# Optimization experiments

Hardware: AMD Instinct MI355X
Metric: run time of the kernel (lower is better)

The kernel has to match this reference:

```python
import jax, jax.numpy as jnp
import numpy as np

N_NODES = 50000
BN_EPS = 1e-5


def sage_conv(x, src, dst, Wl, Wr, b):
    # mean-aggregate neighbor features: message from src -> dst
    msg = x[src]                                             # [E, Din]
    s = jax.ops.segment_sum(msg, dst, num_segments=N_NODES)  # [N, Din]
    cnt = jax.ops.segment_sum(jnp.ones((src.shape[0],), x.dtype), dst,
                              num_segments=N_NODES)          # [N]
    mean = s / jnp.maximum(cnt, 1.0)[:, None]
    # PyG SAGEConv: lin_l(aggregated) (+bias) + lin_r(self), root_weight=True
    return mean @ Wl + b + x @ Wr


def batch_norm(x, gamma, beta):
    mu = jnp.mean(x, axis=0)
    var = jnp.var(x, axis=0)
    return (x - mu) * jax.lax.rsqrt(var + BN_EPS) * gamma + beta


def setup_inputs() -> dict:
    key = jax.random.key(0)
    ks = jax.random.split(key, 16)
    D_IN, D_H, D_OUT = 128, 128, 64
    x = jax.random.normal(ks[0], (N_NODES, D_IN), dtype=jnp.float32)
    edge_index = jax.random.randint(ks[1], (2, 800000), 0, N_NODES, dtype=jnp.int32)

    def xavier(k, din, dout):
        lim = float(np.sqrt(6.0 / (din + dout)))
        return jax.random.uniform(k, (din, dout), jnp.float32, -lim, lim)

    return {
        "x": x, "edge_index": edge_index,
        "Wl0": xavier(ks[2], D_IN, D_H), "Wr0": xavier(ks[3], D_IN, D_H),
        "b0": jnp.zeros((D_H,), jnp.float32),
        "g0": jnp.ones((D_H,), jnp.float32), "be0": jnp.zeros((D_H,), jnp.float32),
        "Wl1": xavier(ks[4], D_H, D_H), "Wr1": xavier(ks[5], D_H, D_H),
        "b1": jnp.zeros((D_H,), jnp.float32),
        "g1": jnp.ones((D_H,), jnp.float32), "be1": jnp.zeros((D_H,), jnp.float32),
        "Wl2": xavier(ks[6], D_H, D_OUT), "Wr2": xavier(ks[7], D_H, D_OUT),
        "b2": jnp.zeros((D_OUT,), jnp.float32),
    }


def reference(x, edge_index, Wl0, Wr0, b0, g0, be0,
              Wl1, Wr1, b1, g1, be1, Wl2, Wr2, b2):
    src, dst = edge_index[0], edge_index[1]
    h = sage_conv(x, src, dst, Wl0, Wr0, b0)
    h = jax.nn.relu(batch_norm(h, g0, be0))
    h = sage_conv(h, src, dst, Wl1, Wr1, b1)
    h = jax.nn.relu(batch_norm(h, g1, be1))
    h = sage_conv(h, src, dst, Wl2, Wr2, b2)
    return jax.nn.log_softmax(h, axis=-1)
```

## Files before the change

kernel.cpp:

```cpp
#include <hip/hip_runtime.h>
#include <hip/hip_bf16.h>

#define D_IN 128
#define D_OUT 64
#define BN_EPS 1e-5f
#define NB_PART 512

typedef short short8 __attribute__((ext_vector_type(8)));
typedef float f32x4 __attribute__((ext_vector_type(4)));
typedef float f32x2 __attribute__((ext_vector_type(2)));
typedef unsigned int u32x4 __attribute__((ext_vector_type(4)));
typedef unsigned int u32x2 __attribute__((ext_vector_type(2)));
typedef unsigned short ushort_t;
typedef unsigned int uint_t;

__device__ __forceinline__ float bf16lo(uint_t v) { return __uint_as_float(v << 16); }
__device__ __forceinline__ float bf16hi(uint_t v) { return __uint_as_float(v & 0xffff0000u); }
__device__ __forceinline__ float bf2f(ushort_t u) { return __uint_as_float(((uint_t)u) << 16); }
__device__ __forceinline__ ushort_t f2bf(float f) {
    union { __hip_bfloat16 h; ushort_t u; } cv;
    cv.h = __float2bfloat16(f);
    return cv.u;
}
__device__ __forceinline__ f32x4 ntload4(const float* p) {
    return __builtin_nontemporal_load((const f32x4*)p);
}


__global__ void hist_kernel(const int* __restrict__ dst, int* __restrict__ cnt, int E) {
    int i = blockIdx.x * 256 + threadIdx.x;
    if (i < E) atomicAdd(&cnt[__builtin_nontemporal_load(&dst[i])], 1);
}

__global__ void scan_part_kernel(const int* __restrict__ cnt, int* __restrict__ bsum, int n) {
    int i = blockIdx.x * 256 + threadIdx.x;
    int v = (i < n) ? cnt[i] : 0;
#pragma unroll
    for (int off = 1; off < 64; off <<= 1) v += __shfl_xor(v, off);
    __shared__ int ws[4];
    int lane = threadIdx.x & 63, wid = threadIdx.x >> 6;
    if (lane == 0) ws[wid] = v;
    __syncthreads();
    if (threadIdx.x == 0) bsum[blockIdx.x] = ws[0] + ws[1] + ws[2] + ws[3];
}

__global__ void scan_mid_kernel(const int* __restrict__ bsum, int* __restrict__ bpre,
                                int* __restrict__ offs, int PB, int n) {
    int t = threadIdx.x;
    int v = (t < PB) ? bsum[t] : 0;
    int lane = t & 63, wid = t >> 6;
    int sc = v;
#pragma unroll
    for (int off = 1; off < 64; off <<= 1) {
        int u = __shfl_up(sc, off);
        if (lane >= off) sc += u;
    }
    __shared__ int ws[4];
    if (lane == 63) ws[wid] = sc;
    __syncthreads();
    int wb = 0;
    for (int w = 0; w < 4; w++) if (w < wid) wb += ws[w];
    int incl = sc + wb;
    if (t < PB) bpre[t] = incl - v;
    if (t == PB - 1) offs[n] = incl;
}

__global__ void scan_final_kernel(const int* __restrict__ cnt, const int* __restrict__ bpre,
                                  int* __restrict__ offs, int* __restrict__ cursor, int n) {
    int b = blockIdx.x, t = threadIdx.x;
    int i = b * 256 + t;
    int v = (i < n) ? cnt[i] : 0;
    int lane = t & 63, wid = t >> 6;
    int sc = v;
#pragma unroll
    for (int off = 1; off < 64; off <<= 1) {
        int u = __shfl_up(sc, off);
        if (lane >= off) sc += u;
    }
    __shared__ int ws[4];
    if (lane == 63) ws[wid] = sc;
    __syncthreads();
    int wb = 0;
    for (int w = 0; w < 4; w++) if (w < wid) wb += ws[w];
    if (i < n) {
        int e = bpre[b] + wb + sc - v;
        offs[i] = e;
        cursor[i] = e;
    }
}

__global__ void scatter_kernel(const int* __restrict__ src, const int* __restrict__ dst,
                               int* __restrict__ cursor, ushort_t* __restrict__ sorted_src,
                               int E, int passW) {
    int lo = blockIdx.y * passW, hi = lo + passW;
    int i = blockIdx.x * 256 + threadIdx.x;
    if (i < E) {
        int d = __builtin_nontemporal_load(&dst[i]);
        if (d >= lo && d < hi) {
            int s = __builtin_nontemporal_load(&src[i]);
            int p = atomicAdd(&cursor[d], 1);
            sorted_src[p] = (ushort_t)s;
        }
    }
}


__global__ void wswz_kernel(const float* __restrict__ Wl0, const float* __restrict__ Wr0,
                            const float* __restrict__ Wl1, const float* __restrict__ Wr1,
                            const float* __restrict__ Wl2, const float* __restrict__ Wr2,
                            short* __restrict__ o0l, short* __restrict__ o0r,
                            short* __restrict__ o1l, short* __restrict__ o1r,
                            short* __restrict__ o2l, short* __restrict__ o2r,
                            int* __restrict__ cnt, int N) {
    int fb = blockIdx.x + 8 * (blockIdx.y + 2 * blockIdx.z);
    for (int i = fb * 256 + threadIdx.x; i < N; i += 48 * 256) cnt[i] = 0;

    int layer = blockIdx.z;
    int Nn = (layer == 2) ? 64 : 128;
    const float* W;
    short* out;
    if (layer == 0) { W = blockIdx.y ? Wr0 : Wl0; out = blockIdx.y ? o0r : o0l; }
    else if (layer == 1) { W = blockIdx.y ? Wr1 : Wl1; out = blockIdx.y ? o1r : o1l; }
    else { W = blockIdx.y ? Wr2 : Wl2; out = blockIdx.y ? o2r : o2l; }
    int g = blockIdx.x * 256 + threadIdx.x;
    int nchunks = (Nn / 16) * 4;
    int chunk = g >> 6, lane = g & 63;
    if (chunk >= nchunks) return;
    int nf = chunk >> 2, kk = chunk & 3;
    short8 s;
#pragma unroll
    for (int j = 0; j < 8; j++) {
        float v = W[(size_t)(kk * 32 + (lane >> 4) * 8 + j) * Nn + nf * 16 + (lane & 15)];
        s[j] = (short)f2bf(v);
    }
    *(short8*)&out[((size_t)(chunk << 6) + lane) * 8] = s;
}


template <int TN, bool BF16IN>
__global__ __launch_bounds__(TN == 128 ? 256 : 128)
void gemm2_mfma(const void* __restrict__ Ain, const short* __restrict__ WlF,
                const short* __restrict__ WrF, ushort_t* __restrict__ Yb,
                ushort_t* __restrict__ Zb, const float* __restrict__ stats,
                const float* __restrict__ gamma, const float* __restrict__ beta, int M) {
    __shared__ short As[64 * 136];
    __shared__ float sc[128], sh[128];
    const int tid = threadIdx.x;
    const int lane = tid & 63;
    const int w = tid >> 6;
    const int row0 = blockIdx.x * 64;
    const int NT = (TN == 128) ? 256 : 128;

    if (BF16IN) {
        if (tid < 128) {
            float invM = 1.0f / (float)M;
            float mu = stats[tid] * invM;
            float var = stats[128 + tid] * invM - mu * mu;
            float scale = gamma[tid] * rsqrtf(var + BN_EPS);
            sc[tid] = scale;
            sh[tid] = beta[tid] - mu * scale;
        }
        __syncthreads();
    }

    for (int c = tid; c < 1024; c += NT) {
        int r = c >> 4, off = (c & 15) * 8;
        short8 v8 = {0, 0, 0, 0, 0, 0, 0, 0};
        if (row0 + r < M) {
            if (BF16IN) {
                const ushort_t* ap = (const ushort_t*)Ain + (size_t)(row0 + r) * 128 + off;
                short8 h = *(const short8*)ap;
#pragma unroll
                for (int j = 0; j < 8; j++) {
                    float f = bf2f((ushort_t)h[j]);
                    f = fmaxf(f * sc[off + j] + sh[off + j], 0.f);
                    v8[j] = (short)f2bf(f);
                }
            } else {
                const float* ap = (const float*)Ain + (size_t)(row0 + r) * 128 + off;
                f32x4 f0 = ntload4(ap);
                f32x4 f1 = ntload4(ap + 4);
#pragma unroll
                for (int j = 0; j < 4; j++) {
                    v8[j] = (short)f2bf(f0[j]);
                    v8[4 + j] = (short)f2bf(f1[j]);
                }
            }
        }
        *(short8*)&As[r * 136 + off] = v8;
    }
    __syncthreads();

    const short* WF;
    ushort_t* D;
    int col0;
    if (TN == 128) {
        bool isY = (w < 2);
        WF = isY ? WlF : WrF;
        D = isY ? Yb : Zb;
        col0 = (w & 1) * 64;
    } else {
        bool isY = (w == 0);
        WF = isY ? WlF : WrF;
        D = isY ? Yb : Zb;
        col0 = 0;
    }

    short8 a[4][4];
#pragma unroll
    for (int m = 0; m < 4; m++)
#pragma unroll
        for (int kk = 0; kk < 4; kk++)
            a[m][kk] = *(const short8*)&As[(m * 16 + (lane & 15)) * 136 + kk * 32 + (lane >> 4) * 8];

    f32x4 acc[4][4];
#pragma unroll
    for (int m = 0; m < 4; m++)
#pragma unroll
        for (int n = 0; n < 4; n++) acc[m][n] = (f32x4){0.f, 0.f, 0.f, 0.f};

#pragma unroll
    for (int kk = 0; kk < 4; kk++) {
#pragma unroll
        for (int n = 0; n < 4; n++) {
            short8 b = *(const short8*)&WF[(size_t)(((col0 >> 4) + n) * 4 + kk) * 512 + lane * 8];
#pragma unroll
            for (int m = 0; m < 4; m++)
                acc[m][n] = __builtin_amdgcn_mfma_f32_16x16x32_bf16(a[m][kk], b, acc[m][n], 0, 0, 0);
        }
    }

#pragma unroll
    for (int m = 0; m < 4; m++) {
#pragma unroll
        for (int i = 0; i < 4; i++) {
            int gr = row0 + m * 16 + (lane >> 4) * 4 + i;
            if (gr < M) {
#pragma unroll
                for (int n = 0; n < 4; n++)
                    D[(size_t)gr * TN + col0 + n * 16 + (lane & 15)] = f2bf(acc[m][n][i]);
            }
        }
    }
}


__global__ __launch_bounds__(256) void agg128_kernel(const ushort_t* __restrict__ Yb,
                                                     const int* __restrict__ offs,
                                                     const ushort_t* __restrict__ sorted_src,
                                                     const float* __restrict__ bias,
                                                     const ushort_t* __restrict__ Zb,
                                                     ushort_t* __restrict__ Hb, int N) {
    int wv = blockIdx.x * 4 + (threadIdx.x >> 6);
    int lane = threadIdx.x & 63;
    int half = lane >> 5, l = lane & 31;
    int node = wv * 2 + half;
    if (node >= N) return;
    int s0 = offs[node], s1 = offs[node + 1];
    float a0 = 0.f, a1 = 0.f, a2 = 0.f, a3 = 0.f;
    int k = s0;
    for (; k + 16 <= s1; k += 16) {
        int idx[16];
#pragma unroll
        for (int j = 0; j < 16; j++) idx[j] = __builtin_nontemporal_load(&sorted_src[k + j]);
        u32x2 v[16];
#pragma unroll
        for (int j = 0; j < 16; j++) v[j] = *(const u32x2*)&Yb[(size_t)idx[j] * 128 + l * 4];
#pragma unroll
        for (int j = 0; j < 16; j++) {
            a0 += bf16lo(v[j][0]);
            a1 += bf16hi(v[j][0]);
            a2 += bf16lo(v[j][1]);
            a3 += bf16hi(v[j][1]);
        }
    }
    for (; k + 4 <= s1; k += 4) {
        int idx[4];
#pragma unroll
        for (int j = 0; j < 4; j++) idx[j] = __builtin_nontemporal_load(&sorted_src[k + j]);
#pragma unroll
        for (int j = 0; j < 4; j++) {
            u32x2 v = *(const u32x2*)&Yb[(size_t)idx[j] * 128 + l * 4];
            a0 += bf16lo(v[0]);
            a1 += bf16hi(v[0]);
            a2 += bf16lo(v[1]);
            a3 += bf16hi(v[1]);
        }
    }
    for (; k < s1; k++) {
        u32x2 v = *(const u32x2*)&Yb[(size_t)sorted_src[k] * 128 + l * 4];
        a0 += bf16lo(v[0]);
        a1 += bf16hi(v[0]);
        a2 += bf16lo(v[1]);
        a3 += bf16hi(v[1]);
    }
    float inv = 1.0f / fmaxf((float)(s1 - s0), 1.0f);
    float4 bb = *(const float4*)&bias[l * 4];
    u32x2 z = __builtin_nontemporal_load((const u32x2*)&Zb[(size_t)node * 128 + l * 4]);
    float h0 = bf16lo(z[0]) + a0 * inv + bb.x;
    float h1 = bf16hi(z[0]) + a1 * inv + bb.y;
    float h2 = bf16lo(z[1]) + a2 * inv + bb.z;
    float h3 = bf16hi(z[1]) + a3 * inv + bb.w;
    u32x2 o;
    o[0] = (uint_t)f2bf(h0) | ((uint_t)f2bf(h1) << 16);
    o[1] = (uint_t)f2bf(h2) | ((uint_t)f2bf(h3) << 16);
    __builtin_nontemporal_store(o, (u32x2*)&Hb[(size_t)node * 128 + l * 4]);
}


__global__ __launch_bounds__(256) void agg_lsm_kernel(const ushort_t* __restrict__ Yb,
                                                      const int* __restrict__ offs,
                                                      const ushort_t* __restrict__ sorted_src,
                                                      const float* __restrict__ bias,
                                                      const ushort_t* __restrict__ Zb,
                                                      float* __restrict__ out, int N) {
    int wv = blockIdx.x * 4 + (threadIdx.x >> 6);
    int lane = threadIdx.x & 63;
    int half = lane >> 5, l = lane & 31;
    int node = wv * 2 + half;
    if (node >= N) return;
    int s0 = offs[node], s1 = offs[node + 1];
    float a0 = 0.f, a1 = 0.f;
    int k = s0;
    for (; k + 8 <= s1; k += 8) {
        int idx[8];
#pragma unroll
        for (int j = 0; j < 8; j++) idx[j] = __builtin_nontemporal_load(&sorted_src[k + j]);
        uint_t v[8];
#pragma unroll
        for (int j = 0; j < 8; j++) v[j] = *(const uint_t*)&Yb[(size_t)idx[j] * 64 + l * 2];
#pragma unroll
        for (int j = 0; j < 8; j++) {
            a0 += bf16lo(v[j]);
            a1 += bf16hi(v[j]);
        }
    }
    for (; k + 4 <= s1; k += 4) {
        int idx[4];
#pragma unroll
        for (int j = 0; j < 4; j++) idx[j] = __builtin_nontemporal_load(&sorted_src[k + j]);
#pragma unroll
        for (int j = 0; j < 4; j++) {
            uint_t v = *(const uint_t*)&Yb[(size_t)idx[j] * 64 + l * 2];
            a0 += bf16lo(v);
            a1 += bf16hi(v);
        }
    }
    for (; k < s1; k++) {
        uint_t v = *(const uint_t*)&Yb[(size_t)sorted_src[k] * 64 + l * 2];
        a0 += bf16lo(v);
        a1 += bf16hi(v);
    }
    float inv = 1.0f / fmaxf((float)(s1 - s0), 1.0f);
    uint_t z = *(const uint_t*)&Zb[(size_t)node * 64 + l * 2];
    float2 bb = *(const float2*)&bias[l * 2];
    float v0 = bf16lo(z) + a0 * inv + bb.x;
    float v1 = bf16hi(z) + a1 * inv + bb.y;
    float m = fmaxf(v0, v1);
#pragma unroll
    for (int off = 16; off; off >>= 1) m = fmaxf(m, __shfl_xor(m, off));
    float s = expf(v0 - m) + expf(v1 - m);
#pragma unroll
    for (int off = 16; off; off >>= 1) s += __shfl_xor(s, off);
    float ls = logf(s);
    f32x2 o;
    o[0] = v0 - m - ls;
    o[1] = v1 - m - ls;
    __builtin_nontemporal_store(o, (f32x2*)&out[(size_t)node * 64 + l * 2]);
}


__global__ __launch_bounds__(256) void bn_part_kernel(const ushort_t* __restrict__ Hb,
                                                      float* __restrict__ P, int M) {
    int b = blockIdx.x;
    int R = (M + NB_PART - 1) / NB_PART;
    int r0 = b * R, r1 = min(r0 + R, M);
    int colg = (threadIdx.x & 15) * 8;
    int rowoff = threadIdx.x >> 4;
    float s[8], s2[8];
#pragma unroll
    for (int j = 0; j < 8; j++) { s[j] = 0.f; s2[j] = 0.f; }
    for (int r = r0 + rowoff; r < r1; r += 16) {
        u32x4 v = __builtin_nontemporal_load((const u32x4*)&Hb[(size_t)r * 128 + colg]);
#pragma unroll
        for (int q = 0; q < 4; q++) {
            float flo = bf16lo(v[q]);
            float fhi = bf16hi(v[q]);
            s[2 * q] += flo;
            s2[2 * q] += flo * flo;
            s[2 * q + 1] += fhi;
            s2[2 * q + 1] += fhi * fhi;
        }
    }
    __shared__ float ls[256][16];
#pragma unroll
    for (int j = 0; j < 8; j++) {
        ls[threadIdx.x][j] = s[j];
        ls[threadIdx.x][8 + j] = s2[j];
    }
    __syncthreads();
    if (threadIdx.x < 128) {
        int g = threadIdx.x >> 3, j = threadIdx.x & 7;
        float a = 0.f, c = 0.f;
#pragma unroll
        for (int kk = 0; kk < 16; kk++) {
            int id = kk * 16 + g;
            a += ls[id][j];
            c += ls[id][8 + j];
        }
        P[(size_t)b * 256 + threadIdx.x] = a;
        P[(size_t)b * 256 + 128 + threadIdx.x] = c;
    }
}

__global__ __launch_bounds__(1024) void bn_reduce_kernel(const float* __restrict__ P,
                                                         float* __restrict__ stats) {
    int c = threadIdx.x & 255, q = threadIdx.x >> 8;
    float acc = 0.f;
#pragma unroll 8
    for (int i = q * (NB_PART / 4); i < (q + 1) * (NB_PART / 4); i++)
        acc += P[(size_t)i * 256 + c];
    __shared__ float ls[4][256];
    ls[q][c] = acc;
    __syncthreads();
    if (threadIdx.x < 256) stats[c] = ls[0][c] + ls[1][c] + ls[2][c] + ls[3][c];
}


extern "C" void kernel_launch(void* const* d_in, const int* in_sizes, int n_in,
                              void* d_out, int out_size, void* d_ws, size_t ws_size,
                              hipStream_t stream) {
    const float* x   = (const float*)d_in[0];
    const int*   ei  = (const int*)d_in[1];
    const float* Wl0 = (const float*)d_in[2];
    const float* Wr0 = (const float*)d_in[3];
    const float* b0  = (const float*)d_in[4];
    const float* g0  = (const float*)d_in[5];
    const float* be0 = (const float*)d_in[6];
    const float* Wl1 = (const float*)d_in[7];
    const float* Wr1 = (const float*)d_in[8];
    const float* b1  = (const float*)d_in[9];
    const float* g1  = (const float*)d_in[10];
    const float* be1 = (const float*)d_in[11];
    const float* Wl2 = (const float*)d_in[12];
    const float* Wr2 = (const float*)d_in[13];
    const float* b2  = (const float*)d_in[14];

    const int N = in_sizes[0] / D_IN;
    const int E = in_sizes[1] / 2;
    const int PB = (N + 255) / 256;

    ushort_t* Hb = (ushort_t*)d_ws;
    ushort_t* Zb = Hb + (size_t)N * D_IN;
    ushort_t* Yb = Zb + (size_t)N * D_IN;
    int* cnt    = (int*)(Yb + (size_t)N * D_IN);
    int* offs   = cnt + N;
    int* cursor = offs + N + 1;
    int* bsum   = cursor + N;
    int* bpre   = bsum + 256;
    ushort_t* sorted = (ushort_t*)(bpre + 256);
    float* stats = (float*)(sorted + E + (E & 1));
    float* P = stats + 512;
    short* WlF0 = (short*)(P + NB_PART * 256);
    short* WrF0 = WlF0 + 16384;
    short* WlF1 = WrF0 + 16384;
    short* WrF1 = WlF1 + 16384;
    short* WlF2 = WrF1 + 16384;
    short* WrF2 = WlF2 + 8192;

    const int eb = (E + 255) / 256;

    wswz_kernel<<<dim3(8, 2, 3), 256, 0, stream>>>(Wl0, Wr0, Wl1, Wr1, Wl2, Wr2,
                                                   WlF0, WrF0, WlF1, WrF1, WlF2, WrF2,
                                                   cnt, N);

    hist_kernel<<<eb, 256, 0, stream>>>(ei + E, cnt, E);
    scan_part_kernel<<<PB, 256, 0, stream>>>(cnt, bsum, N);
    scan_mid_kernel<<<1, 256, 0, stream>>>(bsum, bpre, offs, PB, N);
    scan_final_kernel<<<PB, 256, 0, stream>>>(cnt, bpre, offs, cursor, N);
    scatter_kernel<<<dim3(eb, 2), 256, 0, stream>>>(ei, ei + E, cursor, sorted, E, (N + 1) / 2);

    const int gb = (N + 63) / 64;
    const int ab = (N + 7) / 8;

    gemm2_mfma<128, false><<<gb, 256, 0, stream>>>(x, WlF0, WrF0, Yb, Zb,
                                                   nullptr, nullptr, nullptr, N);
    agg128_kernel<<<ab, 256, 0, stream>>>(Yb, offs, sorted, b0, Zb, Hb, N);
    bn_part_kernel<<<NB_PART, 256, 0, stream>>>(Hb, P, N);
    bn_reduce_kernel<<<1, 1024, 0, stream>>>(P, stats);

    gemm2_mfma<128, true><<<gb, 256, 0, stream>>>(Hb, WlF1, WrF1, Yb, Zb,
                                                  stats, g0, be0, N);
    agg128_kernel<<<ab, 256, 0, stream>>>(Yb, offs, sorted, b1, Zb, Hb, N);
    bn_part_kernel<<<NB_PART, 256, 0, stream>>>(Hb, P, N);
    bn_reduce_kernel<<<1, 1024, 0, stream>>>(P, stats + 256);

    gemm2_mfma<64, true><<<gb, 128, 0, stream>>>(Hb, WlF2, WrF2, Yb, Zb,
                                                 stats + 256, g1, be1, N);
    agg_lsm_kernel<<<ab, 256, 0, stream>>>(Yb, offs, sorted, b2, Zb, (float*)d_out, N);
}
```

Before: 346.4 us.

## Split 128-wide aggregation into column halves across adjacent blocks

The 128-column neighbor aggregation now splits each node's columns into two 64-column halves handled by separate blocks. Block ids are interleaved so that the two halves for the same group of nodes run in adjacent blocks, with each lane loading 4 bytes per neighbor instead of 8. This doubles the number of waves and gives more gather parallelism and latency hiding, and it aims to keep each gathered row half hot in cache for its partner block. The cost is that the index and offset reads are duplicated, and the narrower per-lane loads issue more memory instructions per byte.

```diff
diff --git a/kernel.cpp b/kernel.cpp
--- a/kernel.cpp
+++ b/kernel.cpp
@@ -251,27 +251,30 @@
                                                      const float* __restrict__ bias,
                                                      const ushort_t* __restrict__ Zb,
                                                      ushort_t* __restrict__ Hb, int N) {
-    int wv = blockIdx.x * 4 + (threadIdx.x >> 6);
+    int bid = blockIdx.x;
+    int x = bid & 7;
+    int colhalf = x >> 2;
+    int ng = (bid >> 3) * 4 + (x & 3);
+    int wv = ng * 4 + (threadIdx.x >> 6);
     int lane = threadIdx.x & 63;
     int half = lane >> 5, l = lane & 31;
     int node = wv * 2 + half;
     if (node >= N) return;
+    int cb = colhalf * 64 + l * 2;
     int s0 = offs[node], s1 = offs[node + 1];
-    float a0 = 0.f, a1 = 0.f, a2 = 0.f, a3 = 0.f;
+    float a0 = 0.f, a1 = 0.f;
     int k = s0;
     for (; k + 16 <= s1; k += 16) {
         int idx[16];
 #pragma unroll
         for (int j = 0; j < 16; j++) idx[j] = __builtin_nontemporal_load(&sorted_src[k + j]);
-        u32x2 v[16];
-#pragma unroll
-        for (int j = 0; j < 16; j++) v[j] = *(const u32x2*)&Yb[(size_t)idx[j] * 128 + l * 4];
+        uint_t v[16];
+#pragma unroll
+        for (int j = 0; j < 16; j++) v[j] = *(const uint_t*)&Yb[(size_t)idx[j] * 128 + cb];
 #pragma unroll
         for (int j = 0; j < 16; j++) {
-            a0 += bf16lo(v[j][0]);
-            a1 += bf16hi(v[j][0]);
-            a2 += bf16lo(v[j][1]);
-            a3 += bf16hi(v[j][1]);
+            a0 += bf16lo(v[j]);
+            a1 += bf16hi(v[j]);
         }
     }
     for (; k + 4 <= s1; k += 4) {
@@ -280,31 +283,23 @@
         for (int j = 0; j < 4; j++) idx[j] = __builtin_nontemporal_load(&sorted_src[k + j]);
 #pragma unroll
         for (int j = 0; j < 4; j++) {
-            u32x2 v = *(const u32x2*)&Yb[(size_t)idx[j] * 128 + l * 4];
-            a0 += bf16lo(v[0]);
-            a1 += bf16hi(v[0]);
-            a2 += bf16lo(v[1]);
-            a3 += bf16hi(v[1]);
+            uint_t v = *(const uint_t*)&Yb[(size_t)idx[j] * 128 + cb];
+            a0 += bf16lo(v);
+            a1 += bf16hi(v);
         }
     }
     for (; k < s1; k++) {
-        u32x2 v = *(const u32x2*)&Yb[(size_t)sorted_src[k] * 128 + l * 4];
-        a0 += bf16lo(v[0]);
-        a1 += bf16hi(v[0]);
-        a2 += bf16lo(v[1]);
-        a3 += bf16hi(v[1]);
+        uint_t v = *(const uint_t*)&Yb[(size_t)sorted_src[k] * 128 + cb];
+        a0 += bf16lo(v);
+        a1 += bf16hi(v);
     }
     float inv = 1.0f / fmaxf((float)(s1 - s0), 1.0f);
-    float4 bb = *(const float4*)&bias[l * 4];
-    u32x2 z = __builtin_nontemporal_load((const u32x2*)&Zb[(size_t)node * 128 + l * 4]);
-    float h0 = bf16lo(z[0]) + a0 * inv + bb.x;
-    float h1 = bf16hi(z[0]) + a1 * inv + bb.y;
-    float h2 = bf16lo(z[1]) + a2 * inv + bb.z;
-    float h3 = bf16hi(z[1]) + a3 * inv + bb.w;
-    u32x2 o;
-    o[0] = (uint_t)f2bf(h0) | ((uint_t)f2bf(h1) << 16);
-    o[1] = (uint_t)f2bf(h2) | ((uint_t)f2bf(h3) << 16);
-    __builtin_nontemporal_store(o, (u32x2*)&Hb[(size_t)node * 128 + l * 4]);
+    float2 bb = *(const float2*)&bias[cb];
+    uint_t z = *(const uint_t*)&Zb[(size_t)node * 128 + cb];
+    float h0 = bf16lo(z) + a0 * inv + bb.x;
+    float h1 = bf16hi(z) + a1 * inv + bb.y;
+    uint_t o = (uint_t)f2bf(h0) | ((uint_t)f2bf(h1) << 16);
+    __builtin_nontemporal_store(o, (uint_t*)&Hb[(size_t)node * 128 + cb]);
 }
 
 
@@ -482,16 +477,17 @@
 
     const int gb = (N + 63) / 64;
     const int ab = (N + 7) / 8;
+    const int abx = ((ab + 3) / 4) * 8;
 
     gemm2_mfma<128, false><<<gb, 256, 0, stream>>>(x, WlF0, WrF0, Yb, Zb,
                                                    nullptr, nullptr, nullptr, N);
-    agg128_kernel<<<ab, 256, 0, stream>>>(Yb, offs, sorted, b0, Zb, Hb, N);
+    agg128_kernel<<<abx, 256, 0, stream>>>(Yb, offs, sorted, b0, Zb, Hb, N);
     bn_part_kernel<<<NB_PART, 256, 0, stream>>>(Hb, P, N);
     bn_reduce_kernel<<<1, 1024, 0, stream>>>(P, stats);
 
     gemm2_mfma<128, true><<<gb, 256, 0, stream>>>(Hb, WlF1, WrF1, Yb, Zb,
                                                   stats, g0, be0, N);
-    agg128_kernel<<<ab, 256, 0, stream>>>(Yb, offs, sorted, b1, Zb, Hb, N);
+    agg128_kernel<<<abx, 256, 0, stream>>>(Yb, offs, sorted, b1, Zb, Hb, N);
     bn_part_kernel<<<NB_PART, 256, 0, stream>>>(Hb, P, N);
     bn_reduce_kernel<<<1, 1024, 0, stream>>>(P, stats + 256);
 
```

New measurement: 365.3 us. 1.05x slower.
